# Kernel optimization log

Hardware: AMD Instinct MI355X
Metric: run time of the kernel (lower is better)

The kernel has to match this reference:

```python
import jax, jax.numpy as jnp
import numpy as np

D = 1024
H = 8
DK = D // H
BS, NSEG, NSEN = 16, 64, 32


def _linear_params(key, d_in, d_out, scale=0.02):
    kw, kb = jax.random.split(key)
    w = jax.random.normal(kw, (d_out, d_in), dtype=jnp.float32) * scale
    b = jax.random.normal(kb, (d_out,), dtype=jnp.float32) * scale
    return w, b


def setup_inputs() -> dict:
    key = jax.random.key(0)
    ks = jax.random.split(key, 12)
    A = jax.random.normal(ks[0], (BS, NSEG, D), dtype=jnp.float32)
    V = jax.random.normal(ks[1], (BS, NSEG, D), dtype=jnp.float32)
    S = jax.random.normal(ks[2], (BS, NSEN, D), dtype=jnp.float32)
    wA, bA = _linear_params(ks[3], D, D)
    wV, bV = _linear_params(ks[4], D, D)
    wS, bS = _linear_params(ks[5], D, D)
    wq, bq = _linear_params(ks[6], D, D)
    wk, bk = _linear_params(ks[7], D, D)
    wv, bv = _linear_params(ks[8], D, D)
    w1, b1 = _linear_params(ks[9], D, D)
    w2, b2 = _linear_params(ks[10], D, D)
    return {"A": A, "V": V, "S": S,
            "wA": wA, "bA": bA, "wV": wV, "bV": bV, "wS": wS, "bS": bS,
            "wq": wq, "bq": bq, "wk": wk, "bk": bk, "wv": wv, "bv": bv,
            "w1": w1, "b1": b1, "w2": w2, "b2": b2}


def _lin(x, w, b):
    return x @ w.T + b


def reference(A, V, S, wA, bA, wV, bV, wS, bS, wq, bq, wk, bk, wv, bv, w1, b1, w2, b2):
    bs, num_seg, d_model = A.shape
    num_sen = S.shape[1]
    A = _lin(A, wA, bA)
    V = _lin(V, wV, bV)
    S = _lin(S, wS, bS)
    av = jnp.stack([A, V], axis=2)                       # (bs, num_seg, 2, d)
    q = _lin(S, wq, bq).reshape(bs, num_sen, H, DK)      # (b, s, h, dk)
    k = _lin(av, wk, bk).reshape(bs, num_seg, 2, H, DK)  # (b, g, a, h, dk)
    v = _lin(av, wv, bv).reshape(bs, num_seg, 2, H, DK)
    # attention over the size-2 A/V axis only
    attn = jnp.einsum('bshd,bgahd->bsgah', q, k) / np.sqrt(DK).astype(np.float32)
    attn = jax.nn.softmax(attn, axis=3)                  # softmax over a (A vs V)
    out = jnp.einsum('bsgah,bgahd->bsghd', attn, v)
    out = out.reshape(bs, num_sen, num_seg, d_model)
    # positionwise FF: Linear -> ReLU -> Linear (dropout p=0)
    out = _lin(jax.nn.relu(_lin(out, w1, b1)), w2, b2)
    return out
```

## Files before the change

kernel.cpp:

```cpp
#include <hip/hip_runtime.h>
#include <stdint.h>


#define D_MODEL 1024
#define N_HEAD  8
#define DK      128
#define BS      16
#define NSEG    64
#define NSEN    32

typedef __attribute__((ext_vector_type(8))) __bf16 bf16x8;
typedef __attribute__((ext_vector_type(8))) unsigned short u16x8;
typedef __attribute__((ext_vector_type(4))) float f32x4;

__device__ __forceinline__ float bf2f(unsigned short b) {
  union { unsigned int u; float f; } x; x.u = ((unsigned int)b) << 16; return x.f;
}
__device__ __forceinline__ unsigned short f2bf(float f) {
  union { float f; unsigned int u; } x; x.f = f;
  unsigned int u = x.u;
  unsigned int r = (u + 0x7fffu + ((u >> 16) & 1u)) >> 16;
  return (unsigned short)r;
}

__device__ __forceinline__ void g2l16(const void* g, void* l) {
  __builtin_amdgcn_global_load_lds(
      (const __attribute__((address_space(1))) void*)g,
      (__attribute__((address_space(3))) void*)l, 16, 0, 0);
}

struct CvtB { const float* s[11]; unsigned short* d[11]; int n4[11]; };
__global__ __launch_bounds__(256)
void cvtall_kernel(CvtB p) {
  const int z = blockIdx.y;
  const int i = blockIdx.x * 256 + threadIdx.x;
  if (i >= p.n4[z]) return;
  float4 v = reinterpret_cast<const float4*>(p.s[z])[i];
  ushort4 o;
  o.x = f2bf(v.x); o.y = f2bf(v.y); o.z = f2bf(v.z); o.w = f2bf(v.w);
  reinterpret_cast<ushort4*>(p.d[z])[i] = o;
}

struct GSeg { const unsigned short* A; const unsigned short* B;
              const float* bias; unsigned short* C; };
struct GBatch { GSeg s[3]; int end[3]; };

__global__ __launch_bounds__(256, 4)
void gemm64_bt(GBatch gb) {
  __shared__ __align__(16) unsigned short lds[3 * 6144];

  const int nwg = gridDim.x;
  const int sw = (blockIdx.x & 7) * (nwg >> 3) + (blockIdx.x >> 3);
  int sgi = 0, base = 0;
  if (sw >= gb.end[0]) { sgi = 1; base = gb.end[0]; }
  if (sw >= gb.end[1]) { sgi = 2; base = gb.end[1]; }
  const GSeg sg = gb.s[sgi];
  const int st = sw - base;
  const int m0 = (st >> 3) * 64, n0 = (st & 7) * 128;

  const int t = threadIdx.x;
  const int lane = t & 63, w = t >> 6;
  const int fr = lane & 15, kg = lane >> 4;

  f32x4 acc[2][4] = {};

  const int r  = t >> 2;
  const int c8 = (t & 3) * 8;
  const unsigned short* ga  = sg.A + (size_t)(m0 + r) * 1024 + c8;
  const unsigned short* gbp = sg.B + (size_t)(n0 + r) * 1024 + c8;
  char* ldsc = (char*)lds;

  auto stage = [&](int buf, int k0) {
    char* d = ldsc + buf * 12288;
    g2l16(ga + k0,              d + t * 16);
    g2l16(gbp + k0,             d + 4096 + t * 16);
    g2l16(gbp + k0 + 64 * 1024, d + 8192 + t * 16);
  };

  u16x8 fA[6], fB[6];

#define G64_LOAD(DST, BUF)                                                     \
  {                                                                            \
    const char* bp_ = ldsc + (BUF) * 12288;                                    \
    _Pragma("unroll")                                                          \
    for (int mi = 0; mi < 4; ++mi)                                             \
      DST[mi] = *reinterpret_cast<const u16x8*>(bp_ + (mi * 16 + fr) * 64 + kg * 16); \
    _Pragma("unroll")                                                          \
    for (int ni = 0; ni < 2; ++ni)                                             \
      DST[4 + ni] = *reinterpret_cast<const u16x8*>(bp_ + 4096 + (w * 32 + ni * 16 + fr) * 64 + kg * 16); \
  }

#define G64_MFMA(SRC)                                                          \
  {                                                                            \
    __builtin_amdgcn_s_setprio(1);                                             \
    _Pragma("unroll")                                                          \
    for (int ni = 0; ni < 2; ++ni)                                             \
      _Pragma("unroll")                                                        \
      for (int mi = 0; mi < 4; ++mi)                                           \
        acc[ni][mi] = __builtin_amdgcn_mfma_f32_16x16x32_bf16(                 \
            __builtin_bit_cast(bf16x8, SRC[4 + ni]),                           \
            __builtin_bit_cast(bf16x8, SRC[mi]), acc[ni][mi], 0, 0, 0);        \
    __builtin_amdgcn_s_setprio(0);                                             \
  }

#define G64_ITER(T, CUR, NXT)                                                  \
  {                                                                            \
    if ((T) + 2 < NT) stage(((T) + 2) % 3, ((T) + 2) * 32);                    \
    if ((T) + 1 < NT) {                                                        \
      if ((T) + 2 < NT) asm volatile("s_waitcnt vmcnt(3)" ::: "memory");       \
      else              asm volatile("s_waitcnt vmcnt(0)" ::: "memory");       \
      __builtin_amdgcn_s_barrier();                                            \
      G64_LOAD(NXT, ((T) + 1) % 3);                                            \
    }                                                                          \
    G64_MFMA(CUR);                                                             \
  }

  const int NT = 32;
  stage(0, 0);
  stage(1, 32);
  asm volatile("s_waitcnt vmcnt(3)" ::: "memory");
  __builtin_amdgcn_s_barrier();
  G64_LOAD(fA, 0);

  for (int it = 0; it < NT; it += 2) {
    G64_ITER(it,     fA, fB);
    G64_ITER(it + 1, fB, fA);
  }

#pragma unroll
  for (int ni = 0; ni < 2; ++ni) {
    const int gn0 = n0 + w * 32 + ni * 16 + kg * 4;
    const float4 bv = *reinterpret_cast<const float4*>(&sg.bias[gn0]);
#pragma unroll
    for (int mi = 0; mi < 4; ++mi) {
      const int gm = m0 + mi * 16 + fr;
      ushort4 o;
      o.x = f2bf(acc[ni][mi][0] + bv.x);
      o.y = f2bf(acc[ni][mi][1] + bv.y);
      o.z = f2bf(acc[ni][mi][2] + bv.z);
      o.w = f2bf(acc[ni][mi][3] + bv.w);
      *reinterpret_cast<ushort4*>(&sg.C[(size_t)gm * 1024 + gn0]) = o;
    }
  }
}

__global__ __launch_bounds__(512, 2)
void ff2_gemm(const unsigned short* __restrict__ A, const unsigned short* __restrict__ B,
              const float* __restrict__ bias, float* __restrict__ C,
              int M, int N, int K) {
  __shared__ __align__(16) unsigned short lds[3 * 16384];

  const int nwg = gridDim.x;
  const int sw = (blockIdx.x & 7) * (nwg >> 3) + (blockIdx.x >> 3);
  const int m0 = (sw >> 2) * 256, n0 = (sw & 3) * 256;

  const int T = threadIdx.x;
  const int lane = T & 63, wave = T >> 6;
  const int wr = wave >> 2, wc = wave & 3;
  const int fr = lane & 15, kg = lane >> 4;
  const int NT = K >> 5;

  char* ldsc = (char*)lds;

  const int srow = T >> 2;
  const int gsl = ((T & 3) ^ ((srow & 3) ^ ((srow >> 2) & 3))) * 8;
  const unsigned short* A0 = A + (size_t)(m0 + srow) * K + gsl;
  const unsigned short* A1 = A + (size_t)(m0 + 128 + srow) * K + gsl;
  const unsigned short* B0 = B + (size_t)(n0 + srow) * K + gsl;
  const unsigned short* B1 = B + (size_t)(n0 + 128 + srow) * K + gsl;

  auto stage = [&](int buf, int tt) {
    const int kb = tt * 32;
    char* d = ldsc + buf * 32768 + T * 16;
    g2l16(A0 + kb, d);
    g2l16(A1 + kb, d + 8192);
    g2l16(B0 + kb, d + 16384);
    g2l16(B1 + kb, d + 24576);
  };

  int raddr[8], baddr[4];
#pragma unroll
  for (int mi = 0; mi < 8; ++mi) {
    int ra = wr * 128 + mi * 16 + fr;
    raddr[mi] = ra * 64 + ((kg ^ ((ra & 3) ^ ((ra >> 2) & 3))) * 16);
  }
#pragma unroll
  for (int ni = 0; ni < 4; ++ni) {
    int rb = wc * 64 + ni * 16 + fr;
    baddr[ni] = 16384 + rb * 64 + ((kg ^ ((rb & 3) ^ ((rb >> 2) & 3))) * 16);
  }

  f32x4 acc[4][8] = {};

  u16x8 gA[12], gB[12];

#define FF2_LOAD(DST, BUF)                                                     \
  {                                                                            \
    const char* bp_ = ldsc + (BUF) * 32768;                                    \
    _Pragma("unroll")                                                          \
    for (int mi = 0; mi < 8; ++mi)                                             \
      DST[mi] = *reinterpret_cast<const u16x8*>(bp_ + raddr[mi]);              \
    _Pragma("unroll")                                                          \
    for (int ni = 0; ni < 4; ++ni)                                             \
      DST[8 + ni] = *reinterpret_cast<const u16x8*>(bp_ + baddr[ni]);          \
  }

#define FF2_MFMA(SRC)                                                          \
  {                                                                            \
    __builtin_amdgcn_s_setprio(1);                                             \
    _Pragma("unroll")                                                          \
    for (int ni = 0; ni < 4; ++ni)                                             \
      _Pragma("unroll")                                                        \
      for (int mi = 0; mi < 8; ++mi)                                           \
        acc[ni][mi] = __builtin_amdgcn_mfma_f32_16x16x32_bf16(                 \
            __builtin_bit_cast(bf16x8, SRC[8 + ni]),                           \
            __builtin_bit_cast(bf16x8, SRC[mi]), acc[ni][mi], 0, 0, 0);        \
    __builtin_amdgcn_s_setprio(0);                                             \
  }

#define FF2_ITER(T, CUR, NXT)                                                  \
  {                                                                            \
    if ((T) + 2 < NT) stage(((T) + 2) % 3, (T) + 2);                           \
    if ((T) + 1 < NT) {                                                        \
      if ((T) + 2 < NT) asm volatile("s_waitcnt vmcnt(4)" ::: "memory");       \
      else              asm volatile("s_waitcnt vmcnt(0)" ::: "memory");       \
      __builtin_amdgcn_s_barrier();                                            \
      FF2_LOAD(NXT, ((T) + 1) % 3);                                            \
    }                                                                          \
    FF2_MFMA(CUR);                                                             \
  }

  stage(0, 0);
  stage(1, 1);
  asm volatile("s_waitcnt vmcnt(4)" ::: "memory");
  __builtin_amdgcn_s_barrier();
  FF2_LOAD(gA, 0);

  for (int tt = 0; tt < NT; tt += 2) {
    FF2_ITER(tt,     gA, gB);
    FF2_ITER(tt + 1, gB, gA);
  }

#pragma unroll
  for (int ni = 0; ni < 4; ++ni) {
    const int gn0 = n0 + wc * 64 + ni * 16 + kg * 4;
    const float4 bv = *reinterpret_cast<const float4*>(&bias[gn0]);
#pragma unroll
    for (int mi = 0; mi < 8; ++mi) {
      const int gm = m0 + wr * 128 + mi * 16 + fr;
      float4 o;
      o.x = acc[ni][mi][0] + bv.x;
      o.y = acc[ni][mi][1] + bv.y;
      o.z = acc[ni][mi][2] + bv.z;
      o.w = acc[ni][mi][3] + bv.w;
      *reinterpret_cast<float4*>(&C[(size_t)gm * N + gn0]) = o;
    }
  }
}

__global__ __launch_bounds__(256)
void uav_gemm(const unsigned short* __restrict__ vAV, const unsigned short* __restrict__ w1,
              unsigned short* __restrict__ UAV) {
  __shared__ __align__(16) unsigned short lA[2][128 * 32];
  __shared__ __align__(16) unsigned short lB[2][128 * 32];

  const int zb = blockIdx.z;
  const int tensor = zb >> 3, h = zb & 7;
  const unsigned short* Ab = vAV + (size_t)tensor * (1024 * 1024) + h * 128;
  const unsigned short* Bb = w1 + h * 128;
  unsigned short* Cb = UAV + (size_t)tensor * (1024 * 8192) + h * 1024;

  const int t = threadIdx.x;
  const int m0 = blockIdx.y * 128, n0 = blockIdx.x * 128;
  const int lane = t & 63, wv = t >> 6;
  const int wrow = (wv >> 1) * 64, wcol = (wv & 1) * 64;
  const int fr = lane & 15, kg = lane >> 4;

  f32x4 acc[4][4] = {};

  const int r  = t >> 2;
  const int c8 = (t & 3) * 8;
  const unsigned short* ga = Ab + (size_t)(m0 + r) * 1024 + c8;
  const unsigned short* gb = Bb + (size_t)(n0 + r) * 1024 + c8;

  auto stage = [&](int buf, int k0) {
    g2l16(ga + k0,             &lA[buf][t * 8]);
    g2l16(ga + k0 + 64 * 1024, &lA[buf][2048 + t * 8]);
    g2l16(gb + k0,             &lB[buf][t * 8]);
    g2l16(gb + k0 + 64 * 1024, &lB[buf][2048 + t * 8]);
  };

  stage(0, 0);
  asm volatile("s_waitcnt vmcnt(0)" ::: "memory");
  __syncthreads();

  for (int k0 = 0; k0 < 128; k0 += 32) {
    const int buf = (k0 >> 5) & 1;
    if (k0 + 32 < 128) stage(buf ^ 1, k0 + 32);

    u16x8 af[4], bg_[4];
#pragma unroll
    for (int mi = 0; mi < 4; ++mi)
      af[mi] = *reinterpret_cast<const u16x8*>(&lA[buf][(wrow + mi * 16 + fr) * 32 + kg * 8]);
#pragma unroll
    for (int ni = 0; ni < 4; ++ni)
      bg_[ni] = *reinterpret_cast<const u16x8*>(&lB[buf][(wcol + ni * 16 + fr) * 32 + kg * 8]);
#pragma unroll
    for (int ni = 0; ni < 4; ++ni)
#pragma unroll
      for (int mi = 0; mi < 4; ++mi)
        acc[ni][mi] = __builtin_amdgcn_mfma_f32_16x16x32_bf16(
            __builtin_bit_cast(bf16x8, bg_[ni]), __builtin_bit_cast(bf16x8, af[mi]),
            acc[ni][mi], 0, 0, 0);

    asm volatile("s_waitcnt vmcnt(0)" ::: "memory");
    __syncthreads();
  }

#pragma unroll
  for (int ni = 0; ni < 4; ++ni) {
    const int gn0 = n0 + wcol + ni * 16 + kg * 4;
#pragma unroll
    for (int mi = 0; mi < 4; ++mi) {
      const int gm = m0 + wrow + mi * 16 + fr;
      ushort4 o;
      o.x = f2bf(acc[ni][mi][0]);
      o.y = f2bf(acc[ni][mi][1]);
      o.z = f2bf(acc[ni][mi][2]);
      o.w = f2bf(acc[ni][mi][3]);
      *reinterpret_cast<ushort4*>(&Cb[(size_t)gm * 8192 + gn0]) = o;
    }
  }
}

__global__ __launch_bounds__(256)
void score_hid_kernel(const unsigned short* __restrict__ q,
                      const unsigned short* __restrict__ kAV,
                      const unsigned short* __restrict__ UAV,
                      const float* __restrict__ b1,
                      unsigned short* __restrict__ hid) {
  const int bg = blockIdx.x;
  const int b = bg >> 6, g = bg & 63;
  __shared__ float sk[2][D_MODEL];
  __shared__ float pAl[NSEN][N_HEAD];
  const size_t rowA = (size_t)bg * D_MODEL;
  const size_t rowV = rowA + (size_t)BS * NSEG * D_MODEL;
  for (int i = threadIdx.x; i < D_MODEL; i += 256) {
    sk[0][i] = bf2f(kAV[rowA + i]);
    sk[1][i] = bf2f(kAV[rowV + i]);
  }
  __syncthreads();

  const int h = threadIdx.x >> 5;
  const int l = threadIdx.x & 31;
  const float scale = 0.08838834764831845f;

  for (int s = 0; s < NSEN; ++s) {
    const unsigned short* pq = q + ((size_t)(b * NSEN + s)) * D_MODEL + h * DK;
    float la = 0.f, lv = 0.f;
#pragma unroll
    for (int e = 0; e < 4; ++e) {
      int d = l + e * 32;
      float qv = bf2f(pq[d]);
      la += qv * sk[0][h * DK + d];
      lv += qv * sk[1][h * DK + d];
    }
#pragma unroll
    for (int off = 16; off; off >>= 1) {
      la += __shfl_xor(la, off, 32);
      lv += __shfl_xor(lv, off, 32);
    }
    if (l == 0) pAl[s][h] = 1.f / (1.f + __expf((lv - la) * scale));
  }
  __syncthreads();

  const int n0 = threadIdx.x * 4;
  const unsigned short* ua = UAV + (size_t)bg * 8192 + n0;
  const unsigned short* uv = ua + (size_t)1024 * 8192;

  float dU[N_HEAD][4];
  float base[4];
#pragma unroll
  for (int j = 0; j < 4; ++j) base[j] = b1[n0 + j];
#pragma unroll
  for (int hh = 0; hh < N_HEAD; ++hh) {
    ushort4 a4 = *reinterpret_cast<const ushort4*>(ua + hh * 1024);
    ushort4 v4 = *reinterpret_cast<const ushort4*>(uv + hh * 1024);
    float va[4] = {bf2f(a4.x), bf2f(a4.y), bf2f(a4.z), bf2f(a4.w)};
    float vv[4] = {bf2f(v4.x), bf2f(v4.y), bf2f(v4.z), bf2f(v4.w)};
#pragma unroll
    for (int j = 0; j < 4; ++j) { dU[hh][j] = va[j] - vv[j]; base[j] += vv[j]; }
  }

  for (int s = 0; s < NSEN; ++s) {
    float val[4] = {base[0], base[1], base[2], base[3]};
#pragma unroll
    for (int hh = 0; hh < N_HEAD; ++hh) {
      const float p = pAl[s][hh];
#pragma unroll
      for (int j = 0; j < 4; ++j) val[j] = fmaf(p, dU[hh][j], val[j]);
    }
    ushort4 o;
    o.x = f2bf(val[0] > 0.f ? val[0] : 0.f);
    o.y = f2bf(val[1] > 0.f ? val[1] : 0.f);
    o.z = f2bf(val[2] > 0.f ? val[2] : 0.f);
    o.w = f2bf(val[3] > 0.f ? val[3] : 0.f);
    size_t orow = ((size_t)(b * NSEN + s) * NSEG + g) * D_MODEL + n0;
    *reinterpret_cast<ushort4*>(hid + orow) = o;
  }
}

extern "C" void kernel_launch(void* const* d_in, const int* in_sizes, int n_in,
                              void* d_out, int out_size, void* d_ws, size_t ws_size,
                              hipStream_t stream) {
  const float* A  = (const float*)d_in[0];
  const float* V  = (const float*)d_in[1];
  const float* S  = (const float*)d_in[2];
  const float* wA = (const float*)d_in[3];  const float* bA = (const float*)d_in[4];
  const float* wV = (const float*)d_in[5];  const float* bV = (const float*)d_in[6];
  const float* wS = (const float*)d_in[7];  const float* bS = (const float*)d_in[8];
  const float* wq = (const float*)d_in[9];  const float* bq = (const float*)d_in[10];
  const float* wk = (const float*)d_in[11]; const float* bk = (const float*)d_in[12];
  const float* wv = (const float*)d_in[13]; const float* bv = (const float*)d_in[14];
  const float* w1 = (const float*)d_in[15]; const float* b1 = (const float*)d_in[16];
  const float* w2 = (const float*)d_in[17]; const float* b2 = (const float*)d_in[18];

  const int nAV = BS * NSEG * D_MODEL;
  const int nS  = BS * NSEN * D_MODEL;
  const int nW  = D_MODEL * D_MODEL;
  const int nCT = BS * NSEN * NSEG * D_MODEL;
  const int nU  = 2 * 1024 * 8 * 1024;

  char* ws = (char*)d_ws;
  size_t off = 0;
  auto carve = [&](size_t elems) {
    unsigned short* p = (unsigned short*)(ws + off);
    off += elems * sizeof(unsigned short);
    return p;
  };
  unsigned short* bwA = carve(nW);
  unsigned short* bwV = carve(nW);
  unsigned short* bwS = carve(nW);
  unsigned short* bwq = carve(nW);
  unsigned short* bwk = carve(nW);
  unsigned short* bwv = carve(nW);
  unsigned short* bw1 = carve(nW);
  unsigned short* bw2 = carve(nW);
  unsigned short* xA  = carve(nAV);
  unsigned short* xV  = carve(nAV);
  unsigned short* xS  = carve(nS);
  unsigned short* A1V1 = carve(2 * nAV);
  unsigned short* S1  = carve(nS);
  unsigned short* qb  = carve(nS);
  unsigned short* kAV = carve(2 * nAV);
  unsigned short* vAV = carve(2 * nAV);
  unsigned short* UAV = carve(nU);
  unsigned short* hid = carve(nCT);
  (void)ws_size; (void)n_in; (void)in_sizes; (void)out_size;

  CvtB cv;
  cv.s[0] = wA; cv.d[0] = bwA; cv.n4[0] = nW / 4;
  cv.s[1] = wV; cv.d[1] = bwV; cv.n4[1] = nW / 4;
  cv.s[2] = wS; cv.d[2] = bwS; cv.n4[2] = nW / 4;
  cv.s[3] = wq; cv.d[3] = bwq; cv.n4[3] = nW / 4;
  cv.s[4] = wk; cv.d[4] = bwk; cv.n4[4] = nW / 4;
  cv.s[5] = wv; cv.d[5] = bwv; cv.n4[5] = nW / 4;
  cv.s[6] = w1; cv.d[6] = bw1; cv.n4[6] = nW / 4;
  cv.s[7] = w2; cv.d[7] = bw2; cv.n4[7] = nW / 4;
  cv.s[8] = A;  cv.d[8] = xA;  cv.n4[8] = nAV / 4;
  cv.s[9] = V;  cv.d[9] = xV;  cv.n4[9] = nAV / 4;
  cv.s[10] = S; cv.d[10] = xS; cv.n4[10] = nS / 4;
  cvtall_kernel<<<dim3(1024, 11), dim3(256), 0, stream>>>(cv);

  GBatch pj;
  pj.s[0] = {xA, bwA, bA, A1V1};        pj.end[0] = 128;
  pj.s[1] = {xV, bwV, bV, A1V1 + nAV};  pj.end[1] = 256;
  pj.s[2] = {xS, bwS, bS, S1};          pj.end[2] = 320;
  gemm64_bt<<<dim3(320), 256, 0, stream>>>(pj);

  GBatch qkv;
  qkv.s[0] = {S1,   bwq, bq, qb};   qkv.end[0] = 64;
  qkv.s[1] = {A1V1, bwk, bk, kAV};  qkv.end[1] = 320;
  qkv.s[2] = {A1V1, bwv, bv, vAV};  qkv.end[2] = 576;
  gemm64_bt<<<dim3(576), 256, 0, stream>>>(qkv);

  uav_gemm<<<dim3(8, 8, 16), dim3(256), 0, stream>>>(vAV, bw1, UAV);

  score_hid_kernel<<<dim3(BS * NSEG), dim3(256), 0, stream>>>(qb, kAV, UAV, b1, hid);

  ff2_gemm<<<dim3(512), 512, 0, stream>>>(hid, bw2, b2, (float*)d_out,
                                          32768, 1024, 1024);
}
```

Measured before the change: 202.6 us.

## Switch FF2 GEMM to 32x32 MFMA, deepen gemm64 pipeline, widen hidden stores

The FF2 GEMM moves from 16x16x32 to 32x32x16 bf16 MFMA tiles, with remapped LDS read addresses and a new epilogue, which cuts instruction count and raises operand reuse per wave. gemm64_bt goes from a 3-stage to a 4-stage LDS pipeline with adjusted vmcnt waits, trading occupancy (launch bounds 4 to 3) for deeper latency hiding. The hidden-activation kernel now has each thread handle 8 columns and half the sentences, giving 16-byte stores. The new 32x32 layout mapping and the wait counts carry correctness risk.

After: 214.3 us. 5.8% more time.

```diff
diff --git a/kernel.cpp b/kernel.cpp
--- a/kernel.cpp
+++ b/kernel.cpp
@@ -12,6 +12,7 @@
 typedef __attribute__((ext_vector_type(8))) __bf16 bf16x8;
 typedef __attribute__((ext_vector_type(8))) unsigned short u16x8;
 typedef __attribute__((ext_vector_type(4))) float f32x4;
+typedef __attribute__((ext_vector_type(16))) float f32x16;
 
 __device__ __forceinline__ float bf2f(unsigned short b) {
   union { unsigned int u; float f; } x; x.u = ((unsigned int)b) << 16; return x.f;
@@ -45,9 +46,9 @@
               const float* bias; unsigned short* C; };
 struct GBatch { GSeg s[3]; int end[3]; };
 
-__global__ __launch_bounds__(256, 4)
+__global__ __launch_bounds__(256, 3)
 void gemm64_bt(GBatch gb) {
-  __shared__ __align__(16) unsigned short lds[3 * 6144];
+  __shared__ __align__(16) unsigned short lds[4 * 6144];
 
   const int nwg = gridDim.x;
   const int sw = (blockIdx.x & 7) * (nwg >> 3) + (blockIdx.x >> 3);
@@ -105,12 +106,13 @@
 
 #define G64_ITER(T, CUR, NXT)                                                  \
   {                                                                            \
-    if ((T) + 2 < NT) stage(((T) + 2) % 3, ((T) + 2) * 32);                    \
+    if ((T) + 3 < NT) stage(((T) + 3) & 3, ((T) + 3) * 32);                    \
     if ((T) + 1 < NT) {                                                        \
-      if ((T) + 2 < NT) asm volatile("s_waitcnt vmcnt(3)" ::: "memory");       \
-      else              asm volatile("s_waitcnt vmcnt(0)" ::: "memory");       \
+      if ((T) + 3 < NT)      asm volatile("s_waitcnt vmcnt(6)" ::: "memory");  \
+      else if ((T) + 2 < NT) asm volatile("s_waitcnt vmcnt(3)" ::: "memory");  \
+      else                   asm volatile("s_waitcnt vmcnt(0)" ::: "memory");  \
       __builtin_amdgcn_s_barrier();                                            \
-      G64_LOAD(NXT, ((T) + 1) % 3);                                            \
+      G64_LOAD(NXT, ((T) + 1) & 3);                                            \
     }                                                                          \
     G64_MFMA(CUR);                                                             \
   }
@@ -118,7 +120,8 @@
   const int NT = 32;
   stage(0, 0);
   stage(1, 32);
-  asm volatile("s_waitcnt vmcnt(3)" ::: "memory");
+  stage(2, 64);
+  asm volatile("s_waitcnt vmcnt(6)" ::: "memory");
   __builtin_amdgcn_s_barrier();
   G64_LOAD(fA, 0);
 
@@ -157,7 +160,7 @@
   const int T = threadIdx.x;
   const int lane = T & 63, wave = T >> 6;
   const int wr = wave >> 2, wc = wave & 3;
-  const int fr = lane & 15, kg = lane >> 4;
+  const int l31 = lane & 31, lh = lane >> 5;
   const int NT = K >> 5;
 
   char* ldsc = (char*)lds;
@@ -180,17 +183,23 @@
 
   int raddr[8], baddr[4];
 #pragma unroll
-  for (int mi = 0; mi < 8; ++mi) {
-    int ra = wr * 128 + mi * 16 + fr;
-    raddr[mi] = ra * 64 + ((kg ^ ((ra & 3) ^ ((ra >> 2) & 3))) * 16);
-  }
-#pragma unroll
-  for (int ni = 0; ni < 4; ++ni) {
-    int rb = wc * 64 + ni * 16 + fr;
-    baddr[ni] = 16384 + rb * 64 + ((kg ^ ((rb & 3) ^ ((rb >> 2) & 3))) * 16);
-  }
-
-  f32x4 acc[4][8] = {};
+  for (int mt = 0; mt < 4; ++mt)
+#pragma unroll
+    for (int kk = 0; kk < 2; ++kk) {
+      int ra = wr * 128 + mt * 32 + l31;
+      int slot = (kk * 2 + lh) ^ ((ra & 3) ^ ((ra >> 2) & 3));
+      raddr[mt * 2 + kk] = ra * 64 + slot * 16;
+    }
+#pragma unroll
+  for (int nt = 0; nt < 2; ++nt)
+#pragma unroll
+    for (int kk = 0; kk < 2; ++kk) {
+      int rb = wc * 64 + nt * 32 + l31;
+      int slot = (kk * 2 + lh) ^ ((rb & 3) ^ ((rb >> 2) & 3));
+      baddr[nt * 2 + kk] = 16384 + rb * 64 + slot * 16;
+    }
+
+  f32x16 acc[2][4] = {};
 
   u16x8 gA[12], gB[12];
 
@@ -198,23 +207,26 @@
   {                                                                            \
     const char* bp_ = ldsc + (BUF) * 32768;                                    \
     _Pragma("unroll")                                                          \
-    for (int mi = 0; mi < 8; ++mi)                                             \
-      DST[mi] = *reinterpret_cast<const u16x8*>(bp_ + raddr[mi]);              \
+    for (int i_ = 0; i_ < 8; ++i_)                                             \
+      DST[i_] = *reinterpret_cast<const u16x8*>(bp_ + raddr[i_]);              \
     _Pragma("unroll")                                                          \
-    for (int ni = 0; ni < 4; ++ni)                                             \
-      DST[8 + ni] = *reinterpret_cast<const u16x8*>(bp_ + baddr[ni]);          \
+    for (int i_ = 0; i_ < 4; ++i_)                                             \
+      DST[8 + i_] = *reinterpret_cast<const u16x8*>(bp_ + baddr[i_]);          \
   }
 
 #define FF2_MFMA(SRC)                                                          \
   {                                                                            \
     __builtin_amdgcn_s_setprio(1);                                             \
     _Pragma("unroll")                                                          \
-    for (int ni = 0; ni < 4; ++ni)                                             \
+    for (int nt = 0; nt < 2; ++nt)                                             \
       _Pragma("unroll")                                                        \
-      for (int mi = 0; mi < 8; ++mi)                                           \
-        acc[ni][mi] = __builtin_amdgcn_mfma_f32_16x16x32_bf16(                 \
-            __builtin_bit_cast(bf16x8, SRC[8 + ni]),                           \
-            __builtin_bit_cast(bf16x8, SRC[mi]), acc[ni][mi], 0, 0, 0);        \
+      for (int mt = 0; mt < 4; ++mt)                                           \
+        _Pragma("unroll")                                                      \
+        for (int kk = 0; kk < 2; ++kk)                                         \
+          acc[nt][mt] = __builtin_amdgcn_mfma_f32_32x32x16_bf16(               \
+              __builtin_bit_cast(bf16x8, SRC[8 + nt * 2 + kk]),                \
+              __builtin_bit_cast(bf16x8, SRC[mt * 2 + kk]),                    \
+              acc[nt][mt], 0, 0, 0);                                           \
     __builtin_amdgcn_s_setprio(0);                                             \
   }
 
@@ -242,20 +254,22 @@
   }
 
 #pragma unroll
-  for (int ni = 0; ni < 4; ++ni) {
-    const int gn0 = n0 + wc * 64 + ni * 16 + kg * 4;
-    const float4 bv = *reinterpret_cast<const float4*>(&bias[gn0]);
-#pragma unroll
-    for (int mi = 0; mi < 8; ++mi) {
-      const int gm = m0 + wr * 128 + mi * 16 + fr;
-      float4 o;
-      o.x = acc[ni][mi][0] + bv.x;
-      o.y = acc[ni][mi][1] + bv.y;
-      o.z = acc[ni][mi][2] + bv.z;
-      o.w = acc[ni][mi][3] + bv.w;
-      *reinterpret_cast<float4*>(&C[(size_t)gm * N + gn0]) = o;
-    }
-  }
+  for (int nt = 0; nt < 2; ++nt)
+#pragma unroll
+    for (int mt = 0; mt < 4; ++mt) {
+      const int gm = m0 + wr * 128 + mt * 32 + l31;
+#pragma unroll
+      for (int q = 0; q < 4; ++q) {
+        const int gn0 = n0 + wc * 64 + nt * 32 + q * 8 + lh * 4;
+        const float4 bv = *reinterpret_cast<const float4*>(&bias[gn0]);
+        float4 o;
+        o.x = acc[nt][mt][q * 4 + 0] + bv.x;
+        o.y = acc[nt][mt][q * 4 + 1] + bv.y;
+        o.z = acc[nt][mt][q * 4 + 2] + bv.z;
+        o.w = acc[nt][mt][q * 4 + 3] + bv.w;
+        *reinterpret_cast<float4*>(&C[(size_t)gm * N + gn0]) = o;
+      }
+    }
 }
 
 __global__ __launch_bounds__(256)
@@ -374,39 +388,41 @@
   }
   __syncthreads();
 
-  const int n0 = threadIdx.x * 4;
-  const unsigned short* ua = UAV + (size_t)bg * 8192 + n0;
+  const int tn = (threadIdx.x & 127) * 8;
+  const int sb = (threadIdx.x >> 7) * 16;
+  const unsigned short* ua = UAV + (size_t)bg * 8192 + tn;
   const unsigned short* uv = ua + (size_t)1024 * 8192;
 
-  float dU[N_HEAD][4];
-  float base[4];
-#pragma unroll
-  for (int j = 0; j < 4; ++j) base[j] = b1[n0 + j];
+  float dU[N_HEAD][8];
+  float base[8];
+#pragma unroll
+  for (int j = 0; j < 8; ++j) base[j] = b1[tn + j];
 #pragma unroll
   for (int hh = 0; hh < N_HEAD; ++hh) {
-    ushort4 a4 = *reinterpret_cast<const ushort4*>(ua + hh * 1024);
-    ushort4 v4 = *reinterpret_cast<const ushort4*>(uv + hh * 1024);
-    float va[4] = {bf2f(a4.x), bf2f(a4.y), bf2f(a4.z), bf2f(a4.w)};
-    float vv[4] = {bf2f(v4.x), bf2f(v4.y), bf2f(v4.z), bf2f(v4.w)};
-#pragma unroll
-    for (int j = 0; j < 4; ++j) { dU[hh][j] = va[j] - vv[j]; base[j] += vv[j]; }
-  }
-
-  for (int s = 0; s < NSEN; ++s) {
-    float val[4] = {base[0], base[1], base[2], base[3]};
+    u16x8 a8 = *reinterpret_cast<const u16x8*>(ua + hh * 1024);
+    u16x8 v8 = *reinterpret_cast<const u16x8*>(uv + hh * 1024);
+#pragma unroll
+    for (int j = 0; j < 8; ++j) {
+      float va = bf2f(a8[j]), vv = bf2f(v8[j]);
+      dU[hh][j] = va - vv; base[j] += vv;
+    }
+  }
+
+  for (int s = sb; s < sb + 16; ++s) {
+    float val[8];
+#pragma unroll
+    for (int j = 0; j < 8; ++j) val[j] = base[j];
 #pragma unroll
     for (int hh = 0; hh < N_HEAD; ++hh) {
       const float p = pAl[s][hh];
 #pragma unroll
-      for (int j = 0; j < 4; ++j) val[j] = fmaf(p, dU[hh][j], val[j]);
-    }
-    ushort4 o;
-    o.x = f2bf(val[0] > 0.f ? val[0] : 0.f);
-    o.y = f2bf(val[1] > 0.f ? val[1] : 0.f);
-    o.z = f2bf(val[2] > 0.f ? val[2] : 0.f);
-    o.w = f2bf(val[3] > 0.f ? val[3] : 0.f);
-    size_t orow = ((size_t)(b * NSEN + s) * NSEG + g) * D_MODEL + n0;
-    *reinterpret_cast<ushort4*>(hid + orow) = o;
+      for (int j = 0; j < 8; ++j) val[j] = fmaf(p, dU[hh][j], val[j]);
+    }
+    u16x8 o;
+#pragma unroll
+    for (int j = 0; j < 8; ++j) o[j] = f2bf(val[j] > 0.f ? val[j] : 0.f);
+    size_t orow = ((size_t)(b * NSEN + s) * NSEG + g) * D_MODEL + tn;
+    *reinterpret_cast<u16x8*>(hid + orow) = o;
   }
 }
 
```
